# Performance work log

Measured on AMD Instinct MI355X. Metric: run time of the kernel, lower is better.

Reference implementation:

```python
import jax, jax.numpy as jnp
import numpy as np

DECAY = 0.999
EPS = 1e-05


def setup_inputs() -> dict:
    key = jax.random.key(0)
    k1, k2 = jax.random.split(key)
    B, L, S, D, E = 32, 8, 512, 256, 2048
    x = jax.random.normal(k1, (B, L, S, D), dtype=jnp.float32)
    # stacked per-quantizer codebooks: embed[l] is the [dim, n_embed] buffer of Quantize l
    embed = jax.random.normal(k2, (L, D, E), dtype=jnp.float32)
    cluster_size = jnp.zeros((L, E), dtype=jnp.float32)
    embed_avg = embed.copy()
    return {"x": x, "embed": embed, "cluster_size": cluster_size, "embed_avg": embed_avg}


def reference(x, embed, cluster_size, embed_avg):
    # x: [B, L, S, D]; embed: [L, D, E]; cluster_size: [L, E]; embed_avg: [L, D, E]
    B, L, S, D = x.shape
    E = embed.shape[-1]

    dist = ((x * x).sum(-1, keepdims=True)
            - 2.0 * jnp.einsum('blsd,lde->blse', x, embed)
            + (embed * embed).sum(1)[None, :, None, :])
    ids = jnp.argmin(dist, axis=-1)  # argmax of -dist == argmin of dist; [B, L, S]

    # codebook lookup: embed_t[l, ids[b,l,s]] -> [B, L, S, D]
    embed_t = jnp.swapaxes(embed, 1, 2)  # [L, E, D]
    q = embed_t[jnp.arange(L)[None, :, None], ids]

    # EMA buffer updates (training mode; done on .data in torch, i.e. no grad)
    l_idx = jnp.broadcast_to(jnp.arange(L)[None, :, None], (B, L, S))
    counts = jnp.zeros((L, E), x.dtype).at[l_idx, ids].add(1.0)  # onehot.sum(0) per quantizer
    embed_sum = jnp.zeros((L, E, D), x.dtype).at[l_idx, ids].add(jax.lax.stop_gradient(x))
    embed_sum = jnp.swapaxes(embed_sum, 1, 2)  # [L, D, E] == flatten.T @ onehot
    new_cluster_size = DECAY * cluster_size + (1.0 - DECAY) * counts
    new_embed_avg = DECAY * embed_avg + (1.0 - DECAY) * embed_sum
    n = new_cluster_size.sum(-1, keepdims=True)  # [L, 1]
    cs = (new_cluster_size + EPS) / (n + E * EPS) * n
    new_embed = new_embed_avg / cs[:, None, :]

    # NOTE: the original loop overwrites `diff` each iteration then does `diff += diff`,
    # so the returned diff is 2 * diff_of_last_quantizer / length (faithfully reproduced).
    diff_last = jnp.mean((jax.lax.stop_gradient(q[:, L - 1]) - x[:, L - 1]) ** 2)
    diff = 2.0 * diff_last / L

    # straight-through estimator
    out = x + jax.lax.stop_gradient(q - x)
    return out, diff, ids, new_embed, new_cluster_size, new_embed_avg
```

## Files before the change

kernel.cpp:

```cpp
#include <hip/hip_runtime.h>

#define LL 8
#define BB 32
#define SS 512
#define DD 256
#define EE 2048
#define LED (LL*DD*EE)
#define LE  (LL*EE)
#define NROWS (BB*LL*SS)
#define NKS 17

typedef __bf16 bf16x8 __attribute__((ext_vector_type(8)));
typedef float  f32x16 __attribute__((ext_vector_type(16)));

__global__ void transpose_norms_kernel(const float* __restrict__ embed,
                                       float* __restrict__ embed_t,
                                       float* __restrict__ norms) {
    __shared__ float tile[32][33];
    const int l  = blockIdx.z;
    const int d0 = blockIdx.y * 32;
    const int e0 = blockIdx.x * 32;
    const int tx = threadIdx.x, ty = threadIdx.y;

    float v = embed[((size_t)l*DD + d0 + ty)*EE + e0 + tx];
    tile[ty][tx] = v;
    __syncthreads();
    embed_t[((size_t)l*EE + e0 + ty)*DD + d0 + tx] = tile[tx][ty];
    __syncthreads();
    tile[ty][tx] = v * v;
    __syncthreads();
    if (ty == 0) {
        float s = 0.f;
        #pragma unroll
        for (int i = 0; i < 32; ++i) s += tile[i][tx];
        atomicAdd(&norms[l*EE + e0 + tx], s);
    }
}

__global__ void prep_embed_frag(const float* __restrict__ embed,
                                const float* __restrict__ norms,
                                __bf16* __restrict__ frag) {
    const int bid   = blockIdx.x;
    const int kstep = bid % NKS;
    const int mtile = (bid / NKS) % 64;
    const int l     = bid / (NKS * 64);
    const int lane  = threadIdx.x;
    const int e     = mtile*32 + (lane & 31);
    const int kbase = kstep*16 + (lane >> 5)*8;

    bf16x8 vh, vl;
    if (kstep < 16) {
        #pragma unroll
        for (int j = 0; j < 8; ++j) {
            float v = embed[((size_t)l*DD + kbase + j)*EE + e];
            __bf16 h = (__bf16)v;
            vh[j] = h;
            vl[j] = (__bf16)(v - (float)h);
        }
    } else {
        #pragma unroll
        for (int j = 0; j < 8; ++j) { vh[j] = (__bf16)0.0f; vl[j] = (__bf16)0.0f; }
        if (kbase == 256) {
            float nv = -0.5f * norms[l*EE + e];
            __bf16 ch = (__bf16)nv;
            vh[0] = ch;
            vh[1] = (__bf16)(nv - (float)ch);
        }
    }
    size_t base = ((((size_t)l*64 + mtile)*2 + 0)*NKS + kstep)*64 + lane;
    *(bf16x8*)(frag + base*8) = vh;
    base = ((((size_t)l*64 + mtile)*2 + 1)*NKS + kstep)*64 + lane;
    *(bf16x8*)(frag + base*8) = vl;
}

__global__ __launch_bounds__(256, 2)
void argmin_mfma(const float* __restrict__ x,
                 const __bf16* __restrict__ frag,
                 const float* __restrict__ embed_t,
                 int* __restrict__ ids_out,
                 int* __restrict__ counts_i,
                 float* __restrict__ out,
                 float* __restrict__ diff_acc) {
    __shared__ __bf16 smem[2][2*NKS*512];

    const int tid  = threadIdx.x;
    const int wave = tid >> 6, lane = tid & 63;
    const int l    = blockIdx.x & 7;
    const int rb   = blockIdx.x >> 3;
    const int idx  = rb*4 + wave;
    const int b    = idx >> 4, st = idx & 15;
    const int rowtile = (b*LL + l)*16 + st;

    bf16x8 bh[NKS], bl[16];
    {
        const float* xr = x + (size_t)(rowtile*32 + (lane & 31))*DD + (lane >> 5)*8;
        #pragma unroll
        for (int ks = 0; ks < 16; ++ks) {
            float4 v0 = *(const float4*)(xr + ks*16);
            float4 v1 = *(const float4*)(xr + ks*16 + 4);
            float f[8] = {v0.x, v0.y, v0.z, v0.w, v1.x, v1.y, v1.z, v1.w};
            #pragma unroll
            for (int j = 0; j < 8; ++j) {
                __bf16 h = (__bf16)f[j];
                bh[ks][j] = h;
                bl[ks][j] = (__bf16)(f[j] - (float)h);
            }
        }
        #pragma unroll
        for (int j = 0; j < 8; ++j) bh[16][j] = (__bf16)0.0f;
        if (lane < 32) { bh[16][0] = (__bf16)1.0f; bh[16][1] = (__bf16)1.0f; }
    }

    const __bf16* fl = frag + (size_t)l*64*2*NKS*512;

    auto stage = [&](int m, int buf) {
        const __bf16* src = fl + (size_t)m*2*NKS*512;
        __bf16* dst = &smem[buf][0];
        for (int i = wave; i < 2*NKS; i += 4) {
            __builtin_amdgcn_global_load_lds(
                (const __attribute__((address_space(1))) void*)(src + i*512 + lane*8),
                (__attribute__((address_space(3))) void*)(dst + i*512), 16, 0, 0);
        }
    };

    float maxv = -3.4e38f;
    int   maxi = 0;

    stage(0, 0);
    __syncthreads();
    for (int m = 0; m < 64; ++m) {
        const int buf = m & 1;
        if (m < 63) stage(m + 1, buf ^ 1);
        const __bf16* sA = &smem[buf][0];
        f32x16 a0, a1, a2;
        #pragma unroll
        for (int i = 0; i < 16; ++i) { a0[i] = 0.0f; a1[i] = 0.0f; a2[i] = 0.0f; }
        #pragma unroll
        for (int ks = 0; ks < 16; ++ks) {
            bf16x8 ah = *(const bf16x8*)(sA + ks*512 + lane*8);
            bf16x8 al = *(const bf16x8*)(sA + (NKS + ks)*512 + lane*8);
            a0 = __builtin_amdgcn_mfma_f32_32x32x16_bf16(ah, bh[ks], a0, 0, 0, 0);
            a1 = __builtin_amdgcn_mfma_f32_32x32x16_bf16(ah, bl[ks], a1, 0, 0, 0);
            a2 = __builtin_amdgcn_mfma_f32_32x32x16_bf16(al, bh[ks], a2, 0, 0, 0);
        }
        {
            bf16x8 ah = *(const bf16x8*)(sA + 16*512 + lane*8);
            a0 = __builtin_amdgcn_mfma_f32_32x32x16_bf16(ah, bh[16], a0, 0, 0, 0);
        }
        const int ebase = m*32 + 4*(lane >> 5);
        #pragma unroll
        for (int r = 0; r < 16; ++r) {
            float v = a0[r] + a1[r] + a2[r];
            int e = ebase + (r & 3) + 8*(r >> 2);
            if (v > maxv) { maxv = v; maxi = e; }
        }
        __syncthreads();
    }
    float ov = __shfl_xor(maxv, 32, 64);
    int   oi = __shfl_xor(maxi, 32, 64);
    if (ov > maxv || (ov == maxv && oi < maxi)) { maxv = ov; maxi = oi; }
    if (lane < 32) {
        ids_out[(size_t)rowtile*32 + lane] = maxi;
        atomicAdd(&counts_i[l*EE + maxi], 1);
    }

    const float4* et4  = (const float4*)embed_t;
    const float4* x4   = (const float4*)x;
    float4*       out4 = (float4*)out;
    float sq = 0.f;
    #pragma unroll 4
    for (int r = 0; r < 32; ++r) {
        int id = __shfl(maxi, r);
        float4 qv = et4[((size_t)l*EE + id)*64 + lane];
        size_t o = ((size_t)rowtile*32 + r)*64 + lane;
        out4[o] = qv;
        if (l == LL - 1) {
            float4 xv = x4[o];
            float dx = qv.x - xv.x, dy = qv.y - xv.y, dz = qv.z - xv.z, dw = qv.w - xv.w;
            sq += dx*dx + dy*dy + dz*dz + dw*dw;
        }
    }
    if (l == LL - 1) {
        #pragma unroll
        for (int off = 32; off; off >>= 1) sq += __shfl_down(sq, off);
        if (lane == 0) atomicAdd(diff_acc, sq);
    }
}

__global__ __launch_bounds__(256)
void scan_kernel(const int* __restrict__ counts_i,
                 const float* __restrict__ cs_in,
                 int* __restrict__ bin_start,
                 int* __restrict__ cursor,
                 float* __restrict__ ncs_out,
                 float* __restrict__ n_out) {
    __shared__ int part[256];
    __shared__ float red[4];
    const int l = blockIdx.x, tid = threadIdx.x;
    const int base = l*EE + tid*8;
    int local[8], tsum = 0;
    float fsum = 0.f;
    #pragma unroll
    for (int j = 0; j < 8; ++j) {
        local[j] = counts_i[base + j];
        tsum += local[j];
        float v = 0.999f*cs_in[base + j] + 0.001f*(float)local[j];
        ncs_out[base + j] = v;
        fsum += v;
    }
    part[tid] = tsum;
    __syncthreads();
    for (int off = 1; off < 256; off <<= 1) {
        int v = (tid >= off) ? part[tid - off] : 0;
        __syncthreads();
        part[tid] += v;
        __syncthreads();
    }
    int run = part[tid] - tsum;
    #pragma unroll
    for (int j = 0; j < 8; ++j) {
        bin_start[base + j] = run;
        cursor[base + j]    = run;
        run += local[j];
    }
    #pragma unroll
    for (int off = 32; off; off >>= 1) fsum += __shfl_down(fsum, off);
    if ((tid & 63) == 0) red[tid >> 6] = fsum;
    __syncthreads();
    if (tid == 0) n_out[l] = red[0] + red[1] + red[2] + red[3];
}

__global__ __launch_bounds__(256)
void scatter_idx_kernel(const int* __restrict__ ids,
                        int* __restrict__ cursor,
                        int* __restrict__ sorted_rows) {
    const int r = blockIdx.x*256 + threadIdx.x;
    const int l = (r >> 9) & 7;
    const int e = ids[r];
    int pos = atomicAdd(&cursor[l*EE + e], 1);
    sorted_rows[l*(NROWS/LL) + pos] = r;
}

__global__ __launch_bounds__(256)
void segsum_kernel(const float* __restrict__ x,
                   const int* __restrict__ sorted_rows,
                   const int* __restrict__ bin_start,
                   const int* __restrict__ counts_i,
                   float* __restrict__ embed_sum) {
    const int bid = blockIdx.x;
    const int l   = bid >> 11;
    const int e   = bid & 2047;
    const int tid = threadIdx.x;
    const int start = bin_start[l*EE + e];
    const int cnt   = counts_i[l*EE + e];
    const int* rows = sorted_rows + l*(NROWS/LL);

    float acc = 0.f;
    int i = 0;
    for (; i + 1 < cnt; i += 2) {
        int r0 = rows[start + i], r1 = rows[start + i + 1];
        acc += x[(size_t)r0*DD + tid] + x[(size_t)r1*DD + tid];
    }
    if (i < cnt) acc += x[(size_t)rows[start + i]*DD + tid];
    embed_sum[((size_t)l*EE + e)*DD + tid] = acc;
}

__global__ void finalize_embed_kernel(const float* __restrict__ embed_avg,
                                      const float* __restrict__ embed_sum,
                                      const float* __restrict__ ncs,
                                      const float* __restrict__ n,
                                      float* __restrict__ nea_out,
                                      float* __restrict__ ne_out) {
    __shared__ float tile[32][33];
    const int l  = blockIdx.z;
    const int d0 = blockIdx.y * 32;
    const int e0 = blockIdx.x * 32;
    const int tx = threadIdx.x, ty = threadIdx.y;

    tile[ty][tx] = embed_sum[((size_t)l*EE + e0 + ty)*DD + d0 + tx];
    __syncthreads();
    const size_t idx = ((size_t)l*DD + d0 + ty)*EE + e0 + tx;
    float nea = 0.999f*embed_avg[idx] + 0.001f*tile[tx][ty];
    nea_out[idx] = nea;
    float nl = n[l];
    float c  = ncs[l*EE + e0 + tx];
    float cs = (c + 1e-5f) / (nl + 0.02048f) * nl;
    ne_out[idx] = nea / cs;
}

__global__ void diff_scale_kernel(const float* __restrict__ diff_acc,
                                  float* __restrict__ diff_out) {
    *diff_out = (*diff_acc / (float)(BB*SS*DD)) * 0.25f;
}

extern "C" void kernel_launch(void* const* d_in, const int* in_sizes, int n_in,
                              void* d_out, int out_size, void* d_ws, size_t ws_size,
                              hipStream_t stream) {
    const float* x            = (const float*)d_in[0];
    const float* embed        = (const float*)d_in[1];
    const float* cluster_size = (const float*)d_in[2];
    const float* embed_avg    = (const float*)d_in[3];

    float* out      = (float*)d_out;
    float* diff_out = out + 33554432;
    int*   ids_out  = (int*)(out + 33554433);
    float* ne_out   = out + 33685505;
    float* ncs_out  = out + 37879809;
    float* nea_out  = out + 37896193;

    float* ws        = (float*)d_ws;
    float* embed_t   = ws;
    float* embed_sum = ws + LED;
    int*   counts_i  = (int*)(ws + 2*(size_t)LED);
    float* norms     = ws + 2*(size_t)LED + LE;
    float* diff_acc  = norms + LE;
    float* n_ws      = diff_acc + 1;
    int*   bin_start = (int*)(n_ws + LL);
    int*   cursor    = bin_start + LE;
    int*   sorted_rows = cursor + LE;
    __bf16* embfrag  = (__bf16*)(sorted_rows + NROWS + 16);

    hipMemsetAsync(counts_i, 0, (size_t)(2*LE + 1) * sizeof(float), stream);

    transpose_norms_kernel<<<dim3(EE/32, DD/32, LL), dim3(32, 32), 0, stream>>>(
        embed, embed_t, norms);

    prep_embed_frag<<<LL*64*NKS, 64, 0, stream>>>(embed, norms, embfrag);

    argmin_mfma<<<1024, 256, 0, stream>>>(x, embfrag, embed_t, ids_out, counts_i,
                                          out, diff_acc);

    scan_kernel<<<LL, 256, 0, stream>>>(counts_i, cluster_size, bin_start, cursor,
                                        ncs_out, n_ws);

    scatter_idx_kernel<<<NROWS/256, 256, 0, stream>>>(ids_out, cursor, sorted_rows);

    segsum_kernel<<<LE, 256, 0, stream>>>(x, sorted_rows, bin_start, counts_i, embed_sum);

    finalize_embed_kernel<<<dim3(EE/32, DD/32, LL), dim3(32, 32), 0, stream>>>(
        embed_avg, embed_sum, ncs_out, n_ws, nea_out, ne_out);

    diff_scale_kernel<<<1, 1, 0, stream>>>(diff_acc, diff_out);
}
```

Baseline: 960.1 us.

## Pipeline codebook staging in half-tiles with fine-grained waitcnt barriers

Reorganizes the precomputed bf16 hi/lo codebook fragments into 33 contiguous segments per tile, so each 32-code tile can be loaded in two halves. The argmin kernel now runs a finer software pipeline: it issues the next half-tile's global-to-LDS loads while computing the current half, and replaces __syncthreads with explicit vmcnt waits plus s_barrier. MFMA issue is grouped into phases raised with s_setprio. The goal is to hide LDS staging latency and cut full-block sync stalls, at the cost of fragile hand-tuned vmcnt counts and dummy loads into a scratch area.

```diff
diff --git a/kernel.cpp b/kernel.cpp
--- a/kernel.cpp
+++ b/kernel.cpp
@@ -9,6 +9,7 @@
 #define LE  (LL*EE)
 #define NROWS (BB*LL*SS)
 #define NKS 17
+#define NSEG 33
 
 typedef __bf16 bf16x8 __attribute__((ext_vector_type(8)));
 typedef float  f32x16 __attribute__((ext_vector_type(16)));
@@ -40,37 +41,35 @@
 __global__ void prep_embed_frag(const float* __restrict__ embed,
                                 const float* __restrict__ norms,
                                 __bf16* __restrict__ frag) {
-    const int bid   = blockIdx.x;
-    const int kstep = bid % NKS;
-    const int mtile = (bid / NKS) % 64;
-    const int l     = bid / (NKS * 64);
-    const int lane  = threadIdx.x;
-    const int e     = mtile*32 + (lane & 31);
-    const int kbase = kstep*16 + (lane >> 5)*8;
-
-    bf16x8 vh, vl;
-    if (kstep < 16) {
-        #pragma unroll
-        for (int j = 0; j < 8; ++j) {
-            float v = embed[((size_t)l*DD + kbase + j)*EE + e];
-            __bf16 h = (__bf16)v;
-            vh[j] = h;
-            vl[j] = (__bf16)(v - (float)h);
-        }
-    } else {
-        #pragma unroll
-        for (int j = 0; j < 8; ++j) { vh[j] = (__bf16)0.0f; vl[j] = (__bf16)0.0f; }
-        if (kbase == 256) {
+    const int bid  = blockIdx.x;
+    const int s    = bid % NSEG;
+    const int m    = (bid / NSEG) % 64;
+    const int l    = bid / (NSEG * 64);
+    const int lane = threadIdx.x;
+    const int e    = m*32 + (lane & 31);
+
+    bf16x8 v;
+    if (s == NSEG - 1) {
+        #pragma unroll
+        for (int j = 0; j < 8; ++j) v[j] = (__bf16)0.0f;
+        if ((lane >> 5) == 0) {
             float nv = -0.5f * norms[l*EE + e];
             __bf16 ch = (__bf16)nv;
-            vh[0] = ch;
-            vh[1] = (__bf16)(nv - (float)ch);
-        }
-    }
-    size_t base = ((((size_t)l*64 + mtile)*2 + 0)*NKS + kstep)*64 + lane;
-    *(bf16x8*)(frag + base*8) = vh;
-    base = ((((size_t)l*64 + mtile)*2 + 1)*NKS + kstep)*64 + lane;
-    *(bf16x8*)(frag + base*8) = vl;
+            v[0] = ch;
+            v[1] = (__bf16)(nv - (float)ch);
+        }
+    } else {
+        const bool lo = (s >= 8 && s < 16) || (s >= 24);
+        const int ks  = (s < 8) ? s : (s < 16) ? s - 8 : (s < 24) ? s - 8 : s - 16;
+        const int kbase = ks*16 + (lane >> 5)*8;
+        #pragma unroll
+        for (int j = 0; j < 8; ++j) {
+            float val = embed[((size_t)l*DD + kbase + j)*EE + e];
+            __bf16 h = (__bf16)val;
+            v[j] = lo ? (__bf16)(val - (float)h) : h;
+        }
+    }
+    *(bf16x8*)(frag + (size_t)bid*512 + lane*8) = v;
 }
 
 __global__ __launch_bounds__(256, 2)
@@ -81,7 +80,7 @@
                  int* __restrict__ counts_i,
                  float* __restrict__ out,
                  float* __restrict__ diff_acc) {
-    __shared__ __bf16 smem[2][2*NKS*512];
+    __shared__ __bf16 ldsbuf[66*512 + 512];
 
     const int tid  = threadIdx.x;
     const int wave = tid >> 6, lane = tid & 63;
@@ -111,51 +110,94 @@
         if (lane < 32) { bh[16][0] = (__bf16)1.0f; bh[16][1] = (__bf16)1.0f; }
     }
 
-    const __bf16* fl = frag + (size_t)l*64*2*NKS*512;
-
-    auto stage = [&](int m, int buf) {
-        const __bf16* src = fl + (size_t)m*2*NKS*512;
-        __bf16* dst = &smem[buf][0];
-        for (int i = wave; i < 2*NKS; i += 4) {
+    const __bf16* fl = frag + (size_t)l*64*NSEG*512;
+    __bf16* scratch  = &ldsbuf[66*512];
+
+    auto stage = [&](int u) {
+        const int par   = u & 1;
+        const int nseg  = 16 + par;
+        const bool dmy  = (u >= 128);
+        const int mm    = dmy ? 0 : (u >> 1);
+        const __bf16* src = fl + ((size_t)mm*NSEG + par*16)*512 + lane*8;
+        const int slot  = u & 3;
+        __bf16* dstb = &ldsbuf[((slot >> 1)*33 + (slot & 1)*16)*512];
+        for (int i = wave; i < nseg; i += 4) {
             __builtin_amdgcn_global_load_lds(
-                (const __attribute__((address_space(1))) void*)(src + i*512 + lane*8),
-                (__attribute__((address_space(3))) void*)(dst + i*512), 16, 0, 0);
+                (const __attribute__((address_space(1))) void*)(src + i*512),
+                (__attribute__((address_space(3))) void*)(dmy ? scratch : (dstb + i*512)),
+                16, 0, 0);
         }
     };
 
     float maxv = -3.4e38f;
     int   maxi = 0;
 
-    stage(0, 0);
-    __syncthreads();
-    for (int m = 0; m < 64; ++m) {
-        const int buf = m & 1;
-        if (m < 63) stage(m + 1, buf ^ 1);
-        const __bf16* sA = &smem[buf][0];
-        f32x16 a0, a1, a2;
+    f32x16 a0, a1, a2;
+
+    auto dophase = [&](const __bf16* base, int hi0, int lo0, int ksb) {
+        bf16x8 ah[4], al[4];
+        #pragma unroll
+        for (int k = 0; k < 4; ++k) {
+            ah[k] = *(const bf16x8*)(base + (size_t)(hi0 + k)*512 + lane*8);
+            al[k] = *(const bf16x8*)(base + (size_t)(lo0 + k)*512 + lane*8);
+        }
+        __builtin_amdgcn_s_setprio(1);
+        #pragma unroll
+        for (int k = 0; k < 4; ++k) {
+            a0 = __builtin_amdgcn_mfma_f32_32x32x16_bf16(ah[k], bh[ksb+k], a0, 0, 0, 0);
+            a1 = __builtin_amdgcn_mfma_f32_32x32x16_bf16(ah[k], bl[ksb+k], a1, 0, 0, 0);
+            a2 = __builtin_amdgcn_mfma_f32_32x32x16_bf16(al[k], bh[ksb+k], a2, 0, 0, 0);
+        }
+        __builtin_amdgcn_s_setprio(0);
+    };
+
+    stage(0);
+    stage(1);
+    if (wave == 0) asm volatile("s_waitcnt vmcnt(5)" ::: "memory");
+    else           asm volatile("s_waitcnt vmcnt(4)" ::: "memory");
+    __builtin_amdgcn_s_barrier();
+    __builtin_amdgcn_sched_barrier(0);
+
+    #pragma unroll 1
+    for (int t = 0; t < 64; ++t) {
+        const int u0 = 2*t;
+        const __bf16* A0 = &ldsbuf[(size_t)(t & 1)*(33*512)];
+        const __bf16* A1 = A0 + 16*512;
+
         #pragma unroll
         for (int i = 0; i < 16; ++i) { a0[i] = 0.0f; a1[i] = 0.0f; a2[i] = 0.0f; }
-        #pragma unroll
-        for (int ks = 0; ks < 16; ++ks) {
-            bf16x8 ah = *(const bf16x8*)(sA + ks*512 + lane*8);
-            bf16x8 al = *(const bf16x8*)(sA + (NKS + ks)*512 + lane*8);
-            a0 = __builtin_amdgcn_mfma_f32_32x32x16_bf16(ah, bh[ks], a0, 0, 0, 0);
-            a1 = __builtin_amdgcn_mfma_f32_32x32x16_bf16(ah, bl[ks], a1, 0, 0, 0);
-            a2 = __builtin_amdgcn_mfma_f32_32x32x16_bf16(al, bh[ks], a2, 0, 0, 0);
-        }
+
+        stage(u0 + 2);
+        dophase(A0, 0, 8, 0);
+        __builtin_amdgcn_sched_barrier(0);
+        dophase(A0, 4, 12, 4);
+        asm volatile("s_waitcnt vmcnt(4)" ::: "memory");
+        __builtin_amdgcn_s_barrier();
+        __builtin_amdgcn_sched_barrier(0);
+
+        stage(u0 + 3);
+        dophase(A1, 0, 8, 8);
+        __builtin_amdgcn_sched_barrier(0);
+        dophase(A1, 4, 12, 12);
         {
-            bf16x8 ah = *(const bf16x8*)(sA + 16*512 + lane*8);
-            a0 = __builtin_amdgcn_mfma_f32_32x32x16_bf16(ah, bh[16], a0, 0, 0, 0);
-        }
-        const int ebase = m*32 + 4*(lane >> 5);
+            bf16x8 ahn = *(const bf16x8*)(A1 + (size_t)16*512 + lane*8);
+            a0 = __builtin_amdgcn_mfma_f32_32x32x16_bf16(ahn, bh[16], a0, 0, 0, 0);
+        }
+
+        const int ebase = t*32 + 4*(lane >> 5);
         #pragma unroll
         for (int r = 0; r < 16; ++r) {
             float v = a0[r] + a1[r] + a2[r];
             int e = ebase + (r & 3) + 8*(r >> 2);
             if (v > maxv) { maxv = v; maxi = e; }
         }
-        __syncthreads();
-    }
+
+        if (wave == 0) asm volatile("s_waitcnt vmcnt(5)" ::: "memory");
+        else           asm volatile("s_waitcnt vmcnt(4)" ::: "memory");
+        __builtin_amdgcn_s_barrier();
+        __builtin_amdgcn_sched_barrier(0);
+    }
+
     float ov = __shfl_xor(maxv, 32, 64);
     int   oi = __shfl_xor(maxi, 32, 64);
     if (ov > maxv || (ov == maxv && oi < maxi)) { maxv = ov; maxi = oi; }
@@ -325,7 +367,7 @@
     transpose_norms_kernel<<<dim3(EE/32, DD/32, LL), dim3(32, 32), 0, stream>>>(
         embed, embed_t, norms);
 
-    prep_embed_frag<<<LL*64*NKS, 64, 0, stream>>>(embed, norms, embfrag);
+    prep_embed_frag<<<LL*64*NSEG, 64, 0, stream>>>(embed, norms, embfrag);
 
     argmin_mfma<<<1024, 256, 0, stream>>>(x, embfrag, embed_t, ids_out, counts_i,
                                           out, diff_acc);
```

New measurement: 979.7 us. 2.0% more time.

## Split codebook staging into half-tiles, single accumulator, norms applied from LDS

Applied to the files above, without the earlier changes.

The argmin kernel now stages each codebook tile in two halves through two smaller LDS slots, overlapping the load of one half with MFMA work on the other. The three separate accumulators are merged into one chained accumulator, and the extra MFMA k-step that folded in the norm term is dropped in favour of an fmaf against norms staged in LDS. Shared memory shrinks and launch bounds rise to 3 blocks per CU for more occupancy. The trade-offs are more barriers per tile, a serial MFMA dependency chain on one accumulator, and fp32 rather than bf16-split handling of the norms, which slightly changes rounding.

```diff
diff --git a/kernel.cpp b/kernel.cpp
--- a/kernel.cpp
+++ b/kernel.cpp
@@ -8,7 +8,7 @@
 #define LED (LL*DD*EE)
 #define LE  (LL*EE)
 #define NROWS (BB*LL*SS)
-#define NKS 17
+#define NSEG 32
 
 typedef __bf16 bf16x8 __attribute__((ext_vector_type(8)));
 typedef float  f32x16 __attribute__((ext_vector_type(16)));
@@ -38,50 +38,38 @@
 }
 
 __global__ void prep_embed_frag(const float* __restrict__ embed,
-                                const float* __restrict__ norms,
                                 __bf16* __restrict__ frag) {
-    const int bid   = blockIdx.x;
-    const int kstep = bid % NKS;
-    const int mtile = (bid / NKS) % 64;
-    const int l     = bid / (NKS * 64);
-    const int lane  = threadIdx.x;
-    const int e     = mtile*32 + (lane & 31);
-    const int kbase = kstep*16 + (lane >> 5)*8;
-
-    bf16x8 vh, vl;
-    if (kstep < 16) {
-        #pragma unroll
-        for (int j = 0; j < 8; ++j) {
-            float v = embed[((size_t)l*DD + kbase + j)*EE + e];
-            __bf16 h = (__bf16)v;
-            vh[j] = h;
-            vl[j] = (__bf16)(v - (float)h);
-        }
-    } else {
-        #pragma unroll
-        for (int j = 0; j < 8; ++j) { vh[j] = (__bf16)0.0f; vl[j] = (__bf16)0.0f; }
-        if (kbase == 256) {
-            float nv = -0.5f * norms[l*EE + e];
-            __bf16 ch = (__bf16)nv;
-            vh[0] = ch;
-            vh[1] = (__bf16)(nv - (float)ch);
-        }
-    }
-    size_t base = ((((size_t)l*64 + mtile)*2 + 0)*NKS + kstep)*64 + lane;
-    *(bf16x8*)(frag + base*8) = vh;
-    base = ((((size_t)l*64 + mtile)*2 + 1)*NKS + kstep)*64 + lane;
-    *(bf16x8*)(frag + base*8) = vl;
-}
-
-__global__ __launch_bounds__(256, 2)
+    const int bid  = blockIdx.x;
+    const int s    = bid & 31;
+    const int m    = (bid >> 5) & 63;
+    const int l    = bid >> 11;
+    const int lane = threadIdx.x;
+    const int e    = m*32 + (lane & 31);
+    const int ks   = ((s >> 4) << 3) + ((s & 15) >> 1);
+    const bool lo  = s & 1;
+    const int kbase = ks*16 + (lane >> 5)*8;
+
+    bf16x8 v;
+    #pragma unroll
+    for (int j = 0; j < 8; ++j) {
+        float val = embed[((size_t)l*DD + kbase + j)*EE + e];
+        __bf16 h = (__bf16)val;
+        v[j] = lo ? (__bf16)(val - (float)h) : h;
+    }
+    *(bf16x8*)(frag + (size_t)bid*512 + lane*8) = v;
+}
+
+__global__ __launch_bounds__(256, 3)
 void argmin_mfma(const float* __restrict__ x,
                  const __bf16* __restrict__ frag,
                  const float* __restrict__ embed_t,
+                 const float* __restrict__ norms,
                  int* __restrict__ ids_out,
                  int* __restrict__ counts_i,
                  float* __restrict__ out,
                  float* __restrict__ diff_acc) {
-    __shared__ __bf16 smem[2][2*NKS*512];
+    __shared__ __bf16 slots[2][16*512];
+    __shared__ float  normbuf[EE];
 
     const int tid  = threadIdx.x;
     const int wave = tid >> 6, lane = tid & 63;
@@ -91,7 +79,16 @@
     const int b    = idx >> 4, st = idx & 15;
     const int rowtile = (b*LL + l)*16 + st;
 
-    bf16x8 bh[NKS], bl[16];
+    {
+        const float* np = norms + l*EE;
+        for (int i = wave; i < 8; i += 4) {
+            __builtin_amdgcn_global_load_lds(
+                (const __attribute__((address_space(1))) void*)(np + i*256 + lane*4),
+                (__attribute__((address_space(3))) void*)(normbuf + i*256), 16, 0, 0);
+        }
+    }
+
+    bf16x8 bh[16], bl[16];
     {
         const float* xr = x + (size_t)(rowtile*32 + (lane & 31))*DD + (lane >> 5)*8;
         #pragma unroll
@@ -106,19 +103,16 @@
                 bl[ks][j] = (__bf16)(f[j] - (float)h);
             }
         }
-        #pragma unroll
-        for (int j = 0; j < 8; ++j) bh[16][j] = (__bf16)0.0f;
-        if (lane < 32) { bh[16][0] = (__bf16)1.0f; bh[16][1] = (__bf16)1.0f; }
-    }
-
-    const __bf16* fl = frag + (size_t)l*64*2*NKS*512;
-
-    auto stage = [&](int m, int buf) {
-        const __bf16* src = fl + (size_t)m*2*NKS*512;
-        __bf16* dst = &smem[buf][0];
-        for (int i = wave; i < 2*NKS; i += 4) {
+    }
+
+    const __bf16* fl = frag + (size_t)l*64*NSEG*512;
+
+    auto stage_half = [&](int m, int half, int slot) {
+        const __bf16* src = fl + ((size_t)m*NSEG + half*16)*512 + lane*8;
+        __bf16* dst = &slots[slot][0];
+        for (int i = wave; i < 16; i += 4) {
             __builtin_amdgcn_global_load_lds(
-                (const __attribute__((address_space(1))) void*)(src + i*512 + lane*8),
+                (const __attribute__((address_space(1))) void*)(src + i*512),
                 (__attribute__((address_space(3))) void*)(dst + i*512), 16, 0, 0);
         }
     };
@@ -126,36 +120,52 @@
     float maxv = -3.4e38f;
     int   maxi = 0;
 
-    stage(0, 0);
-    __syncthreads();
-    for (int m = 0; m < 64; ++m) {
-        const int buf = m & 1;
-        if (m < 63) stage(m + 1, buf ^ 1);
-        const __bf16* sA = &smem[buf][0];
-        f32x16 a0, a1, a2;
-        #pragma unroll
-        for (int i = 0; i < 16; ++i) { a0[i] = 0.0f; a1[i] = 0.0f; a2[i] = 0.0f; }
-        #pragma unroll
-        for (int ks = 0; ks < 16; ++ks) {
-            bf16x8 ah = *(const bf16x8*)(sA + ks*512 + lane*8);
-            bf16x8 al = *(const bf16x8*)(sA + (NKS + ks)*512 + lane*8);
-            a0 = __builtin_amdgcn_mfma_f32_32x32x16_bf16(ah, bh[ks], a0, 0, 0, 0);
-            a1 = __builtin_amdgcn_mfma_f32_32x32x16_bf16(ah, bl[ks], a1, 0, 0, 0);
-            a2 = __builtin_amdgcn_mfma_f32_32x32x16_bf16(al, bh[ks], a2, 0, 0, 0);
-        }
-        {
-            bf16x8 ah = *(const bf16x8*)(sA + 16*512 + lane*8);
-            a0 = __builtin_amdgcn_mfma_f32_32x32x16_bf16(ah, bh[16], a0, 0, 0, 0);
-        }
-        const int ebase = m*32 + 4*(lane >> 5);
-        #pragma unroll
-        for (int r = 0; r < 16; ++r) {
-            float v = a0[r] + a1[r] + a2[r];
-            int e = ebase + (r & 3) + 8*(r >> 2);
-            if (v > maxv) { maxv = v; maxi = e; }
+    stage_half(0, 0, 0);
+    __syncthreads();
+
+    #pragma unroll 1
+    for (int t = 0; t < 64; ++t) {
+        stage_half(t, 1, 1);
+
+        f32x16 acc;
+        #pragma unroll
+        for (int i = 0; i < 16; ++i) acc[i] = 0.0f;
+
+        #pragma unroll
+        for (int k = 0; k < 8; ++k) {
+            bf16x8 ah = *(const bf16x8*)(&slots[0][0] + (2*k    )*512 + lane*8);
+            bf16x8 al = *(const bf16x8*)(&slots[0][0] + (2*k + 1)*512 + lane*8);
+            acc = __builtin_amdgcn_mfma_f32_32x32x16_bf16(ah, bh[k], acc, 0, 0, 0);
+            acc = __builtin_amdgcn_mfma_f32_32x32x16_bf16(ah, bl[k], acc, 0, 0, 0);
+            acc = __builtin_amdgcn_mfma_f32_32x32x16_bf16(al, bh[k], acc, 0, 0, 0);
         }
         __syncthreads();
-    }
+
+        if (t < 63) stage_half(t + 1, 0, 0);
+
+        #pragma unroll
+        for (int k = 0; k < 8; ++k) {
+            bf16x8 ah = *(const bf16x8*)(&slots[1][0] + (2*k    )*512 + lane*8);
+            bf16x8 al = *(const bf16x8*)(&slots[1][0] + (2*k + 1)*512 + lane*8);
+            acc = __builtin_amdgcn_mfma_f32_32x32x16_bf16(ah, bh[8+k], acc, 0, 0, 0);
+            acc = __builtin_amdgcn_mfma_f32_32x32x16_bf16(ah, bl[8+k], acc, 0, 0, 0);
+            acc = __builtin_amdgcn_mfma_f32_32x32x16_bf16(al, bh[8+k], acc, 0, 0, 0);
+        }
+
+        const int ebase = t*32 + 4*(lane >> 5);
+        #pragma unroll
+        for (int j = 0; j < 4; ++j) {
+            float4 nv = *(const float4*)(normbuf + t*32 + 8*j + 4*(lane >> 5));
+            #pragma unroll
+            for (int rr = 0; rr < 4; ++rr) {
+                float v = fmaf(-0.5f, (&nv.x)[rr], acc[4*j + rr]);
+                int e = ebase + rr + 8*j;
+                if (v > maxv) { maxv = v; maxi = e; }
+            }
+        }
+        __syncthreads();
+    }
+
     float ov = __shfl_xor(maxv, 32, 64);
     int   oi = __shfl_xor(maxi, 32, 64);
     if (ov > maxv || (ov == maxv && oi < maxi)) { maxv = ov; maxi = oi; }
@@ -325,10 +335,10 @@
     transpose_norms_kernel<<<dim3(EE/32, DD/32, LL), dim3(32, 32), 0, stream>>>(
         embed, embed_t, norms);
 
-    prep_embed_frag<<<LL*64*NKS, 64, 0, stream>>>(embed, norms, embfrag);
-
-    argmin_mfma<<<1024, 256, 0, stream>>>(x, embfrag, embed_t, ids_out, counts_i,
-                                          out, diff_acc);
+    prep_embed_frag<<<LL*64*NSEG, 64, 0, stream>>>(embed, embfrag);
+
+    argmin_mfma<<<1024, 256, 0, stream>>>(x, embfrag, embed_t, norms, ids_out,
+                                          counts_i, out, diff_acc);
 
     scan_kernel<<<LL, 256, 0, stream>>>(counts_i, cluster_size, bin_start, cursor,
                                         ncs_out, n_ws);
```

Result: slower. 1.009 ms (+5.1%).
